# Optimization experiments

Hardware: AMD Instinct MI355X
Metric: run time of the kernel (lower is better)

Reference implementation:

```python
import jax, jax.numpy as jnp
import numpy as np

PATCH_NUMS = (10, 20, 30, 40)   # action_dim=10 * (1,2,3,4)
L = sum(PATCH_NUMS)             # 100
FIRST_L = PATCH_NUMS[0]         # 10
C = 768; NH = 12; HD = C // NH; DEPTH = 8; V = 4096; CVAE = 32; OBS = 23; TO = 1
EPS = 1e-6
STD = 0.02

LVL = np.concatenate([np.full(pn, i, dtype=np.int64) for i, pn in enumerate(PATCH_NUMS)])  # [L]
ATTN_BIAS = np.where(LVL[:, None] >= LVL[None, :], 0.0, -np.inf).astype(np.float32)       # [L, L] block-causal


def _ln(x):
    # LayerNorm without affine (eps=1e-6), as in norm_layer(..., elementwise_affine=False)
    m = x.mean(-1, keepdims=True)
    v = ((x - m) ** 2).mean(-1, keepdims=True)
    return (x - m) / jnp.sqrt(v + EPS)


def setup_inputs() -> dict:
    key = jax.random.key(0)
    ks = iter(jax.random.split(key, 40))
    B = 128
    p = {}
    p["nobs"] = jax.random.normal(next(ks), (B, TO, OBS), jnp.float32)
    p["x_BLCv_wo_first_l"] = jax.random.normal(next(ks), (B, L - FIRST_L, CVAE), jnp.float32)
    p["obs_w"] = jax.random.normal(next(ks), (OBS * TO, C), jnp.float32) * STD
    p["obs_b"] = jnp.zeros((C,), jnp.float32)
    p["word_w"] = jax.random.normal(next(ks), (CVAE, C), jnp.float32) * STD
    p["word_b"] = jnp.zeros((C,), jnp.float32)
    p["pos_start"] = jax.random.normal(next(ks), (1, FIRST_L, C), jnp.float32) * STD
    p["pos_1LC"] = jax.random.normal(next(ks), (1, L, C), jnp.float32) * STD
    p["lvl_emb"] = jax.random.normal(next(ks), (len(PATCH_NUMS), C), jnp.float32) * STD
    p["ada_w"] = jax.random.normal(next(ks), (DEPTH, C, 6 * C), jnp.float32) * STD
    p["ada_b"] = jnp.zeros((DEPTH, 6 * C), jnp.float32)
    p["qkv_w"] = jax.random.normal(next(ks), (DEPTH, C, 3 * C), jnp.float32) * STD
    p["qkv_b"] = jnp.zeros((DEPTH, 3 * C), jnp.float32)
    p["proj_w"] = jax.random.normal(next(ks), (DEPTH, C, C), jnp.float32) * STD
    p["proj_b"] = jnp.zeros((DEPTH, C), jnp.float32)
    p["fc1_w"] = jax.random.normal(next(ks), (DEPTH, C, 4 * C), jnp.float32) * STD
    p["fc1_b"] = jnp.zeros((DEPTH, 4 * C), jnp.float32)
    p["fc2_w"] = jax.random.normal(next(ks), (DEPTH, 4 * C, C), jnp.float32) * STD
    p["fc2_b"] = jnp.zeros((DEPTH, C), jnp.float32)
    p["hnm_w"] = jax.random.normal(next(ks), (C, 2 * C), jnp.float32) * STD
    p["hnm_b"] = jnp.zeros((2 * C,), jnp.float32)
    p["head_w"] = jax.random.normal(next(ks), (C, V), jnp.float32) * STD
    p["head_b"] = jnp.zeros((V,), jnp.float32)
    return p


def reference(nobs, x_BLCv_wo_first_l, obs_w, obs_b, word_w, word_b, pos_start, pos_1LC,
              lvl_emb, ada_w, ada_b, qkv_w, qkv_b, proj_w, proj_b, fc1_w, fc1_b,
              fc2_w, fc2_b, hnm_w, hnm_b, head_w, head_b):
    B = x_BLCv_wo_first_l.shape[0]
    feat = nobs[:, :TO].reshape(B, -1)                     # [B, obs_dim*To]
    cond = feat @ obs_w + obs_b                            # [B, C] (= sos = cond_BD)
    sos = cond[:, None, :] + pos_start                     # [B, first_l, C]
    x = jnp.concatenate([sos, x_BLCv_wo_first_l @ word_w + word_b], axis=1)  # [B, L, C]
    x = x + lvl_emb[jnp.asarray(LVL)][None] + pos_1LC      # lvl + positional embed
    bias = jnp.asarray(ATTN_BIAS)                          # [L, L]
    cond_s = jax.nn.silu(cond)                             # shared SiLU input to each block's ada_lin
    scale = HD ** -0.5
    for i in range(DEPTH):
        ada = (cond_s @ ada_w[i] + ada_b[i]).reshape(B, 1, 6, C)
        g1, g2, s1, s2, sh1, sh2 = (ada[:, :, j] for j in range(6))
        h = _ln(x) * (s1 + 1.0) + sh1
        qkv = (h @ qkv_w[i] + qkv_b[i]).reshape(B, L, 3, NH, HD)
        q, k, v = qkv[:, :, 0], qkv[:, :, 1], qkv[:, :, 2]
        att = jnp.einsum('bqhd,bkhd->bhqk', q, k) * scale
        att = jax.nn.softmax(att + bias, axis=-1)
        o = jnp.einsum('bhqk,bkhd->bqhd', att, v).reshape(B, L, C)
        x = x + (o @ proj_w[i] + proj_b[i]) * g1
        h = _ln(x) * (s2 + 1.0) + sh2
        h = jax.nn.gelu(h @ fc1_w[i] + fc1_b[i]) @ fc2_w[i] + fc2_b[i]
        x = x + h * g2
    # AdaLNBeforeHead + head
    hd = (cond_s @ hnm_w + hnm_b).reshape(B, 1, 2, C)
    x = _ln(x) * (hd[:, :, 0] + 1.0) + hd[:, :, 1]
    return x @ head_w + head_b                             # [B, L, V]
```

## Files before the change

kernel.cpp:

```cpp
#include <hip/hip_runtime.h>
#include <hip/hip_bf16.h>

typedef unsigned short u16;
typedef unsigned int u32;
typedef __attribute__((ext_vector_type(8))) short bf16x8;
typedef __attribute__((ext_vector_type(4))) float f32x4;

#define GLDS(gptr, lptr) __builtin_amdgcn_global_load_lds( \
    (const __attribute__((address_space(1))) u32*)(gptr), \
    (__attribute__((address_space(3))) u32*)(lptr), 16, 0, 0)

__device__ __forceinline__ float bf2f(u16 x) {
  union { float f; u32 u; } c; c.u = ((u32)x) << 16; return c.f;
}
__device__ __forceinline__ u16 f2bf(float f) {
  union { float f; u32 u; } c; c.f = f;
  u32 u = c.u;
  return (u16)((u + 0x7FFFu + ((u >> 16) & 1u)) >> 16);
}

template<int EPI>
__global__ __launch_bounds__(256)
void gemm_kernel(const u16* __restrict__ A, const u16* __restrict__ Bt,
                 const float* __restrict__ bias,
                 u16* __restrict__ outb, float* __restrict__ outf,
                 float* __restrict__ xres, const float* __restrict__ gate, int gstride,
                 int M, int N, int K)
{
  __shared__ u16 ldsA[2][128 * 32];
  __shared__ u16 ldsB[2][128 * 32];
  const int tid = threadIdx.x;
  const int n0 = blockIdx.x * 128;
  const int m0 = blockIdx.y * 128;
  const int wid = tid >> 6, lane = tid & 63;
  const int wm = wid >> 1, wn = wid & 1;
  const int lr = lane & 15, lg = lane >> 4;

  f32x4 acc[4][4];
  #pragma unroll
  for (int i = 0; i < 4; ++i)
    #pragma unroll
    for (int j = 0; j < 4; ++j)
      acc[i][j] = (f32x4){0.f, 0.f, 0.f, 0.f};

  const int KT = K >> 5;
  int cur = 0;

  #define STAGE(buf, kt) do { \
    int k0_ = (kt) << 5; \
    _Pragma("unroll") \
    for (int iss = 0; iss < 2; ++iss) { \
      int f_ = iss * 256 + tid; \
      int row_ = f_ >> 2, gl_ = f_ & 3; \
      int g_ = gl_ ^ (row_ & 3); \
      GLDS(A + (size_t)(m0 + row_) * K + k0_ + g_ * 8, &ldsA[buf][f_ * 8]); \
      GLDS(Bt + (size_t)(n0 + row_) * K + k0_ + g_ * 8, &ldsB[buf][f_ * 8]); \
    } \
  } while (0)

  STAGE(0, 0);
  __syncthreads();
  for (int kt = 0; kt < KT; ++kt) {
    if (kt + 1 < KT) STAGE(cur ^ 1, kt + 1);
    bf16x8 af[4], bfr[4];
    #pragma unroll
    for (int i = 0; i < 4; ++i) {
      int ra = wm * 64 + i * 16 + lr;
      af[i] = *(const bf16x8*)&ldsA[cur][(ra * 4 + (lg ^ (ra & 3))) * 8];
      int rb = wn * 64 + i * 16 + lr;
      bfr[i] = *(const bf16x8*)&ldsB[cur][(rb * 4 + (lg ^ (rb & 3))) * 8];
    }
    #pragma unroll
    for (int mi = 0; mi < 4; ++mi)
      #pragma unroll
      for (int ni = 0; ni < 4; ++ni)
        acc[mi][ni] = __builtin_amdgcn_mfma_f32_16x16x32_bf16(af[mi], bfr[ni], acc[mi][ni], 0, 0, 0);
    __syncthreads();
    cur ^= 1;
  }
  #undef STAGE

  #pragma unroll
  for (int mi = 0; mi < 4; ++mi) {
    #pragma unroll
    for (int ni = 0; ni < 4; ++ni) {
      int col = n0 + wn * 64 + ni * 16 + lr;
      float bcol = bias[col];
      #pragma unroll
      for (int r = 0; r < 4; ++r) {
        int row = m0 + wm * 64 + mi * 16 + lg * 4 + r;
        float v = acc[mi][ni][r] + bcol;
        size_t idx = (size_t)row * N + col;
        if (EPI == 0) {
          outf[idx] = v;
        } else if (EPI == 1) {
          outb[idx] = f2bf(v);
        } else if (EPI == 2) {
          float t = 0.7978845608028654f * (v + 0.044715f * v * v * v);
          t = fminf(fmaxf(t, -15.f), 15.f);
          float e = __expf(2.f * t);
          float g = 0.5f * v * (1.f + (e - 1.f) / (e + 1.f));
          outb[idx] = f2bf(g);
        } else {
          int bb = row / 100;
          float gt = gate[(size_t)bb * gstride + col];
          xres[idx] += v * gt;
        }
      }
    }
  }
}

__global__ __launch_bounds__(256)
void attn_kernel(const u16* __restrict__ qkv, u16* __restrict__ o)
{
  __shared__ u16 Qs[896 * 8];
  __shared__ u16 Ks[896 * 8];
  __shared__ u16 Vt[1024 * 8];
  __shared__ u16 Pl[4][256 * 8];
  const int tid = threadIdx.x;
  const int b = blockIdx.x / 12;
  const int h = blockIdx.x % 12;
  const int wid = tid >> 6, lane = tid & 63;
  const size_t qbase = (size_t)b * 100 * 2304 + h * 64;

  #pragma unroll
  for (int i = 0; i < 16; ++i)
    ((u32*)Pl)[i * 256 + tid] = 0u;

  for (int it = 0; it < 3; ++it) {
    int idx = it * 256 + tid;
    int row = idx >> 3, gl = idx & 7;
    int g = gl ^ (row & 7);
    int sr = row < 100 ? row : 99;
    const u16* gq = qkv + qbase + (size_t)sr * 2304 + g * 8;
    GLDS(gq, &Qs[idx * 8]);
    GLDS(gq + 768, &Ks[idx * 8]);
  }
  if (tid < 128) {
    int idx = 768 + tid;
    int row = idx >> 3, gl = idx & 7;
    int g = gl ^ (row & 7);
    int sr = row < 100 ? row : 99;
    const u16* gq = qkv + qbase + (size_t)sr * 2304 + g * 8;
    GLDS(gq, &Qs[idx * 8]);
    GLDS(gq + 768, &Ks[idx * 8]);
  }

  for (int it = 0; it < 4; ++it) {
    int idx = it * 256 + tid;
    if (idx < 896) {
      int k = idx >> 3, gd = idx & 7;
      int sk = k < 100 ? k : 99;
      const u16* gv = qkv + qbase + (size_t)sk * 2304 + 1536 + gd * 8;
      u16 vv[8];
      *(uint4*)vv = *(const uint4*)gv;
      #pragma unroll
      for (int e = 0; e < 8; ++e) {
        int d = gd * 8 + e;
        Vt[(d * 16 + ((k >> 3) ^ (d & 15))) * 8 + (k & 7)] = vv[e];
      }
    }
  }
  __syncthreads();

  for (int s = wid; s < 7; s += 4) {
    f32x4 sa[7];
    #pragma unroll
    for (int nt = 0; nt < 7; ++nt) sa[nt] = (f32x4){0.f, 0.f, 0.f, 0.f};
    #pragma unroll
    for (int kk = 0; kk < 2; ++kk) {
      int qrow = s * 16 + (lane & 15);
      int qg = kk * 4 + (lane >> 4);
      bf16x8 qa = *(const bf16x8*)&Qs[(qrow * 8 + (qg ^ (qrow & 7))) * 8];
      #pragma unroll
      for (int nt = 0; nt < 7; ++nt) {
        int krow = nt * 16 + (lane & 15);
        bf16x8 kb = *(const bf16x8*)&Ks[(krow * 8 + (qg ^ (krow & 7))) * 8];
        sa[nt] = __builtin_amdgcn_mfma_f32_16x16x32_bf16(qa, kb, sa[nt], 0, 0, 0);
      }
    }
    float pr[7][4];
    #pragma unroll
    for (int r = 0; r < 4; ++r) {
      int q = s * 16 + (lane >> 4) * 4 + r;
      int kmax = q < 10 ? 10 : q < 30 ? 30 : q < 60 ? 60 : 100;
      float m = -1e30f;
      #pragma unroll
      for (int nt = 0; nt < 7; ++nt) {
        int col = nt * 16 + (lane & 15);
        float sv = (col < kmax) ? sa[nt][r] * 0.125f : -1e30f;
        pr[nt][r] = sv;
        m = fmaxf(m, sv);
      }
      m = fmaxf(m, __shfl_xor(m, 1));
      m = fmaxf(m, __shfl_xor(m, 2));
      m = fmaxf(m, __shfl_xor(m, 4));
      m = fmaxf(m, __shfl_xor(m, 8));
      float sum = 0.f;
      #pragma unroll
      for (int nt = 0; nt < 7; ++nt) {
        float e = (pr[nt][r] > -1e29f) ? __expf(pr[nt][r] - m) : 0.f;
        pr[nt][r] = e;
        sum += e;
      }
      sum += __shfl_xor(sum, 1);
      sum += __shfl_xor(sum, 2);
      sum += __shfl_xor(sum, 4);
      sum += __shfl_xor(sum, 8);
      float inv = 1.f / sum;
      #pragma unroll
      for (int nt = 0; nt < 7; ++nt) pr[nt][r] *= inv;
    }
    #pragma unroll
    for (int nt = 0; nt < 7; ++nt) {
      int cg = nt * 2 + ((lane & 15) >> 3);
      int e = lane & 7;
      #pragma unroll
      for (int r = 0; r < 4; ++r) {
        int row = (lane >> 4) * 4 + r;
        Pl[wid][(row * 16 + (cg ^ row)) * 8 + e] = f2bf(pr[nt][r]);
      }
    }
    asm volatile("s_waitcnt lgkmcnt(0)" ::: "memory");
    f32x4 oa[4];
    #pragma unroll
    for (int i = 0; i < 4; ++i) oa[i] = (f32x4){0.f, 0.f, 0.f, 0.f};
    #pragma unroll
    for (int kk = 0; kk < 4; ++kk) {
      int prow = lane & 15;
      int pg = kk * 4 + (lane >> 4);
      bf16x8 pa = *(const bf16x8*)&Pl[wid][(prow * 16 + (pg ^ prow)) * 8];
      #pragma unroll
      for (int nt = 0; nt < 4; ++nt) {
        int vrow = nt * 16 + (lane & 15);
        bf16x8 vb = *(const bf16x8*)&Vt[(vrow * 16 + (pg ^ (vrow & 15))) * 8];
        oa[nt] = __builtin_amdgcn_mfma_f32_16x16x32_bf16(pa, vb, oa[nt], 0, 0, 0);
      }
    }
    #pragma unroll
    for (int nt = 0; nt < 4; ++nt) {
      int d = nt * 16 + (lane & 15);
      #pragma unroll
      for (int r = 0; r < 4; ++r) {
        int q = s * 16 + (lane >> 4) * 4 + r;
        if (q < 100)
          o[(size_t)(b * 100 + q) * 768 + h * 64 + d] = f2bf(oa[nt][r]);
      }
    }
  }
}

__global__ __launch_bounds__(256)
void transpose_cast(const float* __restrict__ in, u16* __restrict__ out, int K, int N)
{
  __shared__ float tile[32][33];
  size_t zo = (size_t)blockIdx.z * K * N;
  const float* ip = in + zo;
  u16* op = out + zo;
  int n0 = blockIdx.x * 32, k0 = blockIdx.y * 32;
  int tx = threadIdx.x & 31, ty = threadIdx.x >> 5;
  #pragma unroll
  for (int i = 0; i < 32; i += 8)
    tile[ty + i][tx] = ip[(size_t)(k0 + ty + i) * N + n0 + tx];
  __syncthreads();
  #pragma unroll
  for (int i = 0; i < 32; i += 8)
    op[(size_t)(n0 + ty + i) * K + k0 + tx] = f2bf(tile[tx][ty + i]);
}

__global__ __launch_bounds__(256)
void cond_kernel(const float* __restrict__ nobs, const float* __restrict__ obs_w,
                 const float* __restrict__ obs_b, float* __restrict__ cond,
                 u16* __restrict__ cond_s)
{
  int idx = blockIdx.x * 256 + threadIdx.x;
  int b = idx / 768, c = idx - b * 768;
  float acc = obs_b[c];
  #pragma unroll
  for (int i = 0; i < 23; ++i)
    acc += nobs[b * 23 + i] * obs_w[i * 768 + c];
  cond[idx] = acc;
  float sg = acc / (1.f + __expf(-acc));
  cond_s[idx] = f2bf(sg);
}

__global__ __launch_bounds__(256)
void cast_bf16_kernel(const float* __restrict__ in, u16* __restrict__ out, int n)
{
  int idx = blockIdx.x * 256 + threadIdx.x;
  if (idx < n) out[idx] = f2bf(in[idx]);
}

__global__ __launch_bounds__(256)
void build_x_kernel(const float* __restrict__ cond, const float* __restrict__ pos_start,
                    const float* __restrict__ xw, const float* __restrict__ lvl_emb,
                    const float* __restrict__ pos_1LC, float* __restrict__ x)
{
  int idx = blockIdx.x * 256 + threadIdx.x;
  int row = idx / 768, c = idx - row * 768;
  int b = row / 100, l = row - b * 100;
  int lvl = l < 10 ? 0 : l < 30 ? 1 : l < 60 ? 2 : 3;
  float v;
  if (l < 10) v = cond[b * 768 + c] + pos_start[l * 768 + c];
  else        v = xw[(size_t)(b * 90 + (l - 10)) * 768 + c];
  x[idx] = v + lvl_emb[lvl * 768 + c] + pos_1LC[l * 768 + c];
}

__global__ __launch_bounds__(256)
void ln_mod_kernel(const float* __restrict__ x, const float* __restrict__ scale_b,
                   const float* __restrict__ shift_b, int stride, u16* __restrict__ h)
{
  int row = blockIdx.x;
  const float* xr = x + (size_t)row * 768;
  int t = threadIdx.x;
  float v0 = xr[t], v1 = xr[t + 256], v2 = xr[t + 512];
  float s = v0 + v1 + v2;
  float q = v0 * v0 + v1 * v1 + v2 * v2;
  #pragma unroll
  for (int o = 32; o > 0; o >>= 1) {
    s += __shfl_down(s, o);
    q += __shfl_down(q, o);
  }
  __shared__ float red[4][2];
  if ((t & 63) == 0) { red[t >> 6][0] = s; red[t >> 6][1] = q; }
  __syncthreads();
  float S = red[0][0] + red[1][0] + red[2][0] + red[3][0];
  float Q = red[0][1] + red[1][1] + red[2][1] + red[3][1];
  float mean = S * (1.f / 768.f);
  float var = Q * (1.f / 768.f) - mean * mean;
  float rstd = rsqrtf(var + 1e-6f);
  int bb = row / 100;
  const float* sc = scale_b + (size_t)bb * stride;
  const float* sh = shift_b + (size_t)bb * stride;
  u16* hr = h + (size_t)row * 768;
  hr[t]       = f2bf((v0 - mean) * rstd * (1.f + sc[t])       + sh[t]);
  hr[t + 256] = f2bf((v1 - mean) * rstd * (1.f + sc[t + 256]) + sh[t + 256]);
  hr[t + 512] = f2bf((v2 - mean) * rstd * (1.f + sc[t + 512]) + sh[t + 512]);
}

extern "C" void kernel_launch(void* const* d_in, const int* in_sizes, int n_in,
                              void* d_out, int out_size, void* d_ws, size_t ws_size,
                              hipStream_t stream)
{
  (void)in_sizes; (void)n_in; (void)out_size; (void)ws_size;
  const float* nobs      = (const float*)d_in[0];
  const float* xv        = (const float*)d_in[1];
  const float* obs_w     = (const float*)d_in[2];
  const float* obs_b     = (const float*)d_in[3];
  const float* word_w    = (const float*)d_in[4];
  const float* word_b    = (const float*)d_in[5];
  const float* pos_start = (const float*)d_in[6];
  const float* pos_1LC   = (const float*)d_in[7];
  const float* lvl_emb   = (const float*)d_in[8];
  const float* ada_w     = (const float*)d_in[9];
  const float* ada_b     = (const float*)d_in[10];
  const float* qkv_w     = (const float*)d_in[11];
  const float* qkv_b     = (const float*)d_in[12];
  const float* proj_w    = (const float*)d_in[13];
  const float* proj_b    = (const float*)d_in[14];
  const float* fc1_w     = (const float*)d_in[15];
  const float* fc1_b     = (const float*)d_in[16];
  const float* fc2_w     = (const float*)d_in[17];
  const float* fc2_b     = (const float*)d_in[18];
  const float* hnm_w     = (const float*)d_in[19];
  const float* hnm_b     = (const float*)d_in[20];
  const float* head_w    = (const float*)d_in[21];
  const float* head_b    = (const float*)d_in[22];
  float* out = (float*)d_out;

  char* p = (char*)d_ws;
  auto take = [&](size_t bytes) { char* r = p; p += (bytes + 255) & ~(size_t)255; return r; };
  u16* Wword   = (u16*)take((size_t)768 * 32 * 2);
  u16* Wada    = (u16*)take((size_t)8 * 4608 * 768 * 2);
  u16* Wqkv    = (u16*)take((size_t)8 * 2304 * 768 * 2);
  u16* Wproj   = (u16*)take((size_t)8 * 768 * 768 * 2);
  u16* Wfc1    = (u16*)take((size_t)8 * 3072 * 768 * 2);
  u16* Wfc2    = (u16*)take((size_t)8 * 768 * 3072 * 2);
  u16* Whnm    = (u16*)take((size_t)1536 * 768 * 2);
  u16* Whead   = (u16*)take((size_t)4096 * 768 * 2);
  float* condf = (float*)take((size_t)128 * 768 * 4);
  u16* conds   = (u16*)take((size_t)128 * 768 * 2);
  u16* xvb     = (u16*)take((size_t)368640 * 2);
  float* xbuf  = (float*)take((size_t)12800 * 768 * 4);
  u16* hbuf    = (u16*)take((size_t)12800 * 768 * 2);
  float* adab  = (float*)take((size_t)128 * 4608 * 4);
  u16* obuf    = (u16*)take((size_t)12800 * 768 * 2);
  float* hdbuf = (float*)take((size_t)128 * 1536 * 4);
  char* big    = take((size_t)12800 * 3072 * 2);
  float* xw  = (float*)big;
  u16* qkvb  = (u16*)big;
  u16* fc1b  = (u16*)big;

  transpose_cast<<<dim3(24, 1, 1),   256, 0, stream>>>(word_w, Wword, 32, 768);
  transpose_cast<<<dim3(144, 24, 8), 256, 0, stream>>>(ada_w,  Wada,  768, 4608);
  transpose_cast<<<dim3(72, 24, 8),  256, 0, stream>>>(qkv_w,  Wqkv,  768, 2304);
  transpose_cast<<<dim3(24, 24, 8),  256, 0, stream>>>(proj_w, Wproj, 768, 768);
  transpose_cast<<<dim3(96, 24, 8),  256, 0, stream>>>(fc1_w,  Wfc1,  768, 3072);
  transpose_cast<<<dim3(24, 96, 8),  256, 0, stream>>>(fc2_w,  Wfc2,  3072, 768);
  transpose_cast<<<dim3(48, 24, 1),  256, 0, stream>>>(hnm_w,  Whnm,  768, 1536);
  transpose_cast<<<dim3(128, 24, 1), 256, 0, stream>>>(head_w, Whead, 768, 4096);

  cond_kernel<<<384, 256, 0, stream>>>(nobs, obs_w, obs_b, condf, conds);
  cast_bf16_kernel<<<1440, 256, 0, stream>>>(xv, xvb, 368640);
  gemm_kernel<0><<<dim3(6, 90), 256, 0, stream>>>(xvb, Wword, word_b,
      nullptr, xw, nullptr, nullptr, 0, 11520, 768, 32);
  build_x_kernel<<<38400, 256, 0, stream>>>(condf, pos_start, xw, lvl_emb, pos_1LC, xbuf);

  for (int i = 0; i < 8; ++i) {
    gemm_kernel<0><<<dim3(36, 1), 256, 0, stream>>>(conds, Wada + (size_t)i * 4608 * 768,
        ada_b + (size_t)i * 4608, nullptr, adab, nullptr, nullptr, 0, 128, 4608, 768);
    ln_mod_kernel<<<12800, 256, 0, stream>>>(xbuf, adab + 2 * 768, adab + 4 * 768, 4608, hbuf);
    gemm_kernel<1><<<dim3(18, 100), 256, 0, stream>>>(hbuf, Wqkv + (size_t)i * 2304 * 768,
        qkv_b + (size_t)i * 2304, qkvb, nullptr, nullptr, nullptr, 0, 12800, 2304, 768);
    attn_kernel<<<1536, 256, 0, stream>>>(qkvb, obuf);
    gemm_kernel<3><<<dim3(6, 100), 256, 0, stream>>>(obuf, Wproj + (size_t)i * 768 * 768,
        proj_b + (size_t)i * 768, nullptr, nullptr, xbuf, adab + 0 * 768, 4608, 12800, 768, 768);
    ln_mod_kernel<<<12800, 256, 0, stream>>>(xbuf, adab + 3 * 768, adab + 5 * 768, 4608, hbuf);
    gemm_kernel<2><<<dim3(24, 100), 256, 0, stream>>>(hbuf, Wfc1 + (size_t)i * 3072 * 768,
        fc1_b + (size_t)i * 3072, fc1b, nullptr, nullptr, nullptr, 0, 12800, 3072, 768);
    gemm_kernel<3><<<dim3(6, 100), 256, 0, stream>>>(fc1b, Wfc2 + (size_t)i * 768 * 3072,
        fc2_b + (size_t)i * 768, nullptr, nullptr, xbuf, adab + 1 * 768, 4608, 12800, 768, 3072);
  }

  gemm_kernel<0><<<dim3(12, 1), 256, 0, stream>>>(conds, Whnm, hnm_b,
      nullptr, hdbuf, nullptr, nullptr, 0, 128, 1536, 768);
  ln_mod_kernel<<<12800, 256, 0, stream>>>(xbuf, hdbuf, hdbuf + 768, 1536, hbuf);
  gemm_kernel<0><<<dim3(32, 100), 256, 0, stream>>>(hbuf, Whead, head_b,
      nullptr, out, nullptr, nullptr, 0, 12800, 4096, 768);
}
```

Baseline: 3.639 ms.

## Add 256x256-tile double-buffered GEMM with XCD remap; batch all adaLN projections

Adds a new GEMM kernel with 256x256 output tiles, 512 threads, 128KB of dynamic LDS double-buffered through global_load_lds, XCD-aware workgroup remapping and setprio around the MFMA bursts. It replaces the previous GEMM for the QKV, proj, fc1, fc2 and head layers. The goal is more data reuse per tile and better overlap of loads with MFMA work. When the workspace is large enough, the eight per-layer adaLN projections are also computed in one launch before the loop, which removes the small GEMM launches inside it. The risks are lower occupancy and the hipFuncSetAttribute call made on every launch.

```diff
diff --git a/kernel.cpp b/kernel.cpp
--- a/kernel.cpp
+++ b/kernel.cpp
@@ -111,6 +111,170 @@
   }
 }
 
+template<int EPI>
+__global__ __launch_bounds__(512, 2)
+void gemm256_kernel(const u16* __restrict__ A, const u16* __restrict__ Bt,
+                    const float* __restrict__ bias,
+                    u16* __restrict__ outb, float* __restrict__ outf,
+                    float* __restrict__ xres, const float* __restrict__ gate, int gstride,
+                    int M, int N, int K)
+{
+  extern __shared__ u16 lds[];
+  u16* ldsA = lds;
+  u16* ldsB = lds + 32768;
+  const int tid = threadIdx.x;
+  const int nX = N >> 8;
+
+  int nwg = gridDim.x;
+  int orig = blockIdx.x;
+  int q = nwg >> 3, r = nwg & 7;
+  int xcd = orig & 7, jj = orig >> 3;
+  int wg = (xcd < r ? xcd * (q + 1) : r * (q + 1) + (xcd - r) * q) + jj;
+  const int m0 = (wg / nX) << 8;
+  const int n0 = (wg % nX) << 8;
+
+  const int wid = tid >> 6, lane = tid & 63;
+  const int wm = wid >> 2, wn = wid & 3;
+  const int lr = lane & 15, lg = lane >> 4;
+
+  const u16* Ag = A + (size_t)m0 * K;
+  const u16* Bg = Bt + (size_t)n0 * K;
+
+  f32x4 acc[8][4];
+  #pragma unroll
+  for (int i = 0; i < 8; ++i)
+    #pragma unroll
+    for (int j = 0; j < 4; ++j)
+      acc[i][j] = (f32x4){0.f, 0.f, 0.f, 0.f};
+
+  const int KT = K >> 6;
+
+  #define ISSUE(ldsbase, G, buf, t1, kk) do { \
+    int k0_ = ((t1) << 6) + ((kk) << 5); \
+    _Pragma("unroll") \
+    for (int is_ = 0; is_ < 2; ++is_) { \
+      int j_ = is_ * 512 + tid; \
+      int row_ = j_ >> 2, gl_ = j_ & 3; \
+      int gs_ = gl_ ^ (row_ & 3); \
+      GLDS((G) + (size_t)row_ * K + k0_ + gs_ * 8, \
+           (ldsbase) + (((((buf) * 2 + (kk)) << 10)) + j_) * 8); \
+    } \
+  } while (0)
+
+  #define RDA(dst, buf, kk, mf) do { \
+    int r_ = wm * 128 + (mf) * 16 + lr; \
+    dst = *(const bf16x8*)&ldsA[(((((buf) * 2 + (kk)) << 10)) + r_ * 4 + (lg ^ (r_ & 3))) * 8]; \
+  } while (0)
+  #define RDB(dst, buf, kk, nf) do { \
+    int r_ = wn * 64 + (nf) * 16 + lr; \
+    dst = *(const bf16x8*)&ldsB[(((((buf) * 2 + (kk)) << 10)) + r_ * 4 + (lg ^ (r_ & 3))) * 8]; \
+  } while (0)
+
+  ISSUE(ldsA, Ag, 0, 0, 0);
+  ISSUE(ldsB, Bg, 0, 0, 0);
+  ISSUE(ldsA, Ag, 0, 0, 1);
+  ISSUE(ldsB, Bg, 0, 0, 1);
+
+  for (int t = 0; t < KT; ++t) {
+    const int c = t & 1;
+    const bool pf = (t + 1) < KT;
+    bf16x8 af[4], bv[4];
+
+    asm volatile("s_waitcnt vmcnt(4)" ::: "memory");
+    __builtin_amdgcn_s_barrier();
+    if (pf) { ISSUE(ldsA, Ag, c ^ 1, t + 1, 0); }
+    RDA(af[0], c, 0, 0); RDA(af[1], c, 0, 1); RDA(af[2], c, 0, 2); RDA(af[3], c, 0, 3);
+    RDB(bv[0], c, 0, 0); RDB(bv[1], c, 0, 1); RDB(bv[2], c, 0, 2); RDB(bv[3], c, 0, 3);
+    __builtin_amdgcn_s_setprio(1);
+    #pragma unroll
+    for (int i = 0; i < 4; ++i)
+      #pragma unroll
+      for (int j = 0; j < 4; ++j)
+        acc[i][j] = __builtin_amdgcn_mfma_f32_16x16x32_bf16(af[i], bv[j], acc[i][j], 0, 0, 0);
+    __builtin_amdgcn_s_setprio(0);
+
+    __builtin_amdgcn_s_barrier();
+    if (pf) { ISSUE(ldsB, Bg, c ^ 1, t + 1, 0); }
+    RDA(af[0], c, 0, 4); RDA(af[1], c, 0, 5); RDA(af[2], c, 0, 6); RDA(af[3], c, 0, 7);
+    __builtin_amdgcn_s_setprio(1);
+    #pragma unroll
+    for (int i = 0; i < 4; ++i)
+      #pragma unroll
+      for (int j = 0; j < 4; ++j)
+        acc[4 + i][j] = __builtin_amdgcn_mfma_f32_16x16x32_bf16(af[i], bv[j], acc[4 + i][j], 0, 0, 0);
+    __builtin_amdgcn_s_setprio(0);
+
+    if (pf) { asm volatile("s_waitcnt vmcnt(4)" ::: "memory"); }
+    else    { asm volatile("s_waitcnt vmcnt(0)" ::: "memory"); }
+    __builtin_amdgcn_s_barrier();
+    if (pf) { ISSUE(ldsA, Ag, c ^ 1, t + 1, 1); }
+    RDA(af[0], c, 1, 0); RDA(af[1], c, 1, 1); RDA(af[2], c, 1, 2); RDA(af[3], c, 1, 3);
+    RDB(bv[0], c, 1, 0); RDB(bv[1], c, 1, 1); RDB(bv[2], c, 1, 2); RDB(bv[3], c, 1, 3);
+    __builtin_amdgcn_s_setprio(1);
+    #pragma unroll
+    for (int i = 0; i < 4; ++i)
+      #pragma unroll
+      for (int j = 0; j < 4; ++j)
+        acc[i][j] = __builtin_amdgcn_mfma_f32_16x16x32_bf16(af[i], bv[j], acc[i][j], 0, 0, 0);
+    __builtin_amdgcn_s_setprio(0);
+
+    __builtin_amdgcn_s_barrier();
+    if (pf) { ISSUE(ldsB, Bg, c ^ 1, t + 1, 1); }
+    RDA(af[0], c, 1, 4); RDA(af[1], c, 1, 5); RDA(af[2], c, 1, 6); RDA(af[3], c, 1, 7);
+    __builtin_amdgcn_s_setprio(1);
+    #pragma unroll
+    for (int i = 0; i < 4; ++i)
+      #pragma unroll
+      for (int j = 0; j < 4; ++j)
+        acc[4 + i][j] = __builtin_amdgcn_mfma_f32_16x16x32_bf16(af[i], bv[j], acc[4 + i][j], 0, 0, 0);
+    __builtin_amdgcn_s_setprio(0);
+  }
+  #undef ISSUE
+  #undef RDA
+  #undef RDB
+
+  #pragma unroll
+  for (int nf = 0; nf < 4; ++nf) {
+    int col = n0 + wn * 64 + nf * 16 + lr;
+    float bcol = bias[col];
+    #pragma unroll
+    for (int mf = 0; mf < 8; ++mf) {
+      #pragma unroll
+      for (int r = 0; r < 4; ++r) {
+        int row = m0 + wm * 128 + mf * 16 + lg * 4 + r;
+        float v = acc[mf][nf][r] + bcol;
+        size_t idx = (size_t)row * N + col;
+        if (EPI == 0) {
+          outf[idx] = v;
+        } else if (EPI == 1) {
+          outb[idx] = f2bf(v);
+        } else if (EPI == 2) {
+          float tg = 0.7978845608028654f * (v + 0.044715f * v * v * v);
+          tg = fminf(fmaxf(tg, -15.f), 15.f);
+          float e = __expf(2.f * tg);
+          float g = 0.5f * v * (1.f + (e - 1.f) / (e + 1.f));
+          outb[idx] = f2bf(g);
+        } else {
+          int bb = row / 100;
+          float gt = gate[(size_t)bb * gstride + col];
+          xres[idx] += v * gt;
+        }
+      }
+    }
+  }
+}
+
+template<int E>
+static inline void launch256(const u16* A, const u16* Bt, const float* bias,
+                             u16* ob, float* of, float* xr, const float* gt, int gs,
+                             int M, int N, int K, hipStream_t s)
+{
+  hipFuncSetAttribute(reinterpret_cast<const void*>(&gemm256_kernel<E>),
+                      hipFuncAttributeMaxDynamicSharedMemorySize, 131072);
+  int nwg = (M >> 8) * (N >> 8);
+  gemm256_kernel<E><<<nwg, 512, 131072, s>>>(A, Bt, bias, ob, of, xr, gt, gs, M, N, K);
+}
+
 __global__ __launch_bounds__(256)
 void attn_kernel(const u16* __restrict__ qkv, u16* __restrict__ o)
 {
@@ -183,8 +347,8 @@
     float pr[7][4];
     #pragma unroll
     for (int r = 0; r < 4; ++r) {
-      int q = s * 16 + (lane >> 4) * 4 + r;
-      int kmax = q < 10 ? 10 : q < 30 ? 30 : q < 60 ? 60 : 100;
+      int qq = s * 16 + (lane >> 4) * 4 + r;
+      int kmax = qq < 10 ? 10 : qq < 30 ? 30 : qq < 60 ? 60 : 100;
       float m = -1e30f;
       #pragma unroll
       for (int nt = 0; nt < 7; ++nt) {
@@ -243,9 +407,9 @@
       int d = nt * 16 + (lane & 15);
       #pragma unroll
       for (int r = 0; r < 4; ++r) {
-        int q = s * 16 + (lane >> 4) * 4 + r;
-        if (q < 100)
-          o[(size_t)(b * 100 + q) * 768 + h * 64 + d] = f2bf(oa[nt][r]);
+        int qq = s * 16 + (lane >> 4) * 4 + r;
+        if (qq < 100)
+          o[(size_t)(b * 100 + qq) * 768 + h * 64 + d] = f2bf(oa[nt][r]);
       }
     }
   }
@@ -316,14 +480,14 @@
   int t = threadIdx.x;
   float v0 = xr[t], v1 = xr[t + 256], v2 = xr[t + 512];
   float s = v0 + v1 + v2;
-  float q = v0 * v0 + v1 * v1 + v2 * v2;
+  float qv = v0 * v0 + v1 * v1 + v2 * v2;
   #pragma unroll
   for (int o = 32; o > 0; o >>= 1) {
     s += __shfl_down(s, o);
-    q += __shfl_down(q, o);
+    qv += __shfl_down(qv, o);
   }
   __shared__ float red[4][2];
-  if ((t & 63) == 0) { red[t >> 6][0] = s; red[t >> 6][1] = q; }
+  if ((t & 63) == 0) { red[t >> 6][0] = s; red[t >> 6][1] = qv; }
   __syncthreads();
   float S = red[0][0] + red[1][0] + red[2][0] + red[3][0];
   float Q = red[0][1] + red[1][1] + red[2][1] + red[3][1];
@@ -343,7 +507,7 @@
                               void* d_out, int out_size, void* d_ws, size_t ws_size,
                               hipStream_t stream)
 {
-  (void)in_sizes; (void)n_in; (void)out_size; (void)ws_size;
+  (void)in_sizes; (void)n_in; (void)out_size;
   const float* nobs      = (const float*)d_in[0];
   const float* xv        = (const float*)d_in[1];
   const float* obs_w     = (const float*)d_in[2];
@@ -369,6 +533,10 @@
   const float* head_b    = (const float*)d_in[22];
   float* out = (float*)d_out;
 
+  const size_t NEED_BIG = 358000000;
+  const bool bigAda = ws_size >= NEED_BIG;
+  const int adaStride = bigAda ? 36864 : 4608;
+
   char* p = (char*)d_ws;
   auto take = [&](size_t bytes) { char* r = p; p += (bytes + 255) & ~(size_t)255; return r; };
   u16* Wword   = (u16*)take((size_t)768 * 32 * 2);
@@ -384,7 +552,7 @@
   u16* xvb     = (u16*)take((size_t)368640 * 2);
   float* xbuf  = (float*)take((size_t)12800 * 768 * 4);
   u16* hbuf    = (u16*)take((size_t)12800 * 768 * 2);
-  float* adab  = (float*)take((size_t)128 * 4608 * 4);
+  float* adab  = (float*)take((size_t)128 * (size_t)adaStride * 4);
   u16* obuf    = (u16*)take((size_t)12800 * 768 * 2);
   float* hdbuf = (float*)take((size_t)128 * 1536 * 4);
   char* big    = take((size_t)12800 * 3072 * 2);
@@ -407,25 +575,31 @@
       nullptr, xw, nullptr, nullptr, 0, 11520, 768, 32);
   build_x_kernel<<<38400, 256, 0, stream>>>(condf, pos_start, xw, lvl_emb, pos_1LC, xbuf);
 
+  if (bigAda)
+    gemm_kernel<0><<<dim3(288, 1), 256, 0, stream>>>(conds, Wada, ada_b,
+        nullptr, adab, nullptr, nullptr, 0, 128, 36864, 768);
+
   for (int i = 0; i < 8; ++i) {
-    gemm_kernel<0><<<dim3(36, 1), 256, 0, stream>>>(conds, Wada + (size_t)i * 4608 * 768,
-        ada_b + (size_t)i * 4608, nullptr, adab, nullptr, nullptr, 0, 128, 4608, 768);
-    ln_mod_kernel<<<12800, 256, 0, stream>>>(xbuf, adab + 2 * 768, adab + 4 * 768, 4608, hbuf);
-    gemm_kernel<1><<<dim3(18, 100), 256, 0, stream>>>(hbuf, Wqkv + (size_t)i * 2304 * 768,
-        qkv_b + (size_t)i * 2304, qkvb, nullptr, nullptr, nullptr, 0, 12800, 2304, 768);
+    if (!bigAda)
+      gemm_kernel<0><<<dim3(36, 1), 256, 0, stream>>>(conds, Wada + (size_t)i * 4608 * 768,
+          ada_b + (size_t)i * 4608, nullptr, adab, nullptr, nullptr, 0, 128, 4608, 768);
+    float* adaL = bigAda ? adab + (size_t)i * 4608 : adab;
+    ln_mod_kernel<<<12800, 256, 0, stream>>>(xbuf, adaL + 2 * 768, adaL + 4 * 768, adaStride, hbuf);
+    launch256<1>(hbuf, Wqkv + (size_t)i * 2304 * 768, qkv_b + (size_t)i * 2304,
+                 qkvb, nullptr, nullptr, nullptr, 0, 12800, 2304, 768, stream);
     attn_kernel<<<1536, 256, 0, stream>>>(qkvb, obuf);
-    gemm_kernel<3><<<dim3(6, 100), 256, 0, stream>>>(obuf, Wproj + (size_t)i * 768 * 768,
-        proj_b + (size_t)i * 768, nullptr, nullptr, xbuf, adab + 0 * 768, 4608, 12800, 768, 768);
-    ln_mod_kernel<<<12800, 256, 0, stream>>>(xbuf, adab + 3 * 768, adab + 5 * 768, 4608, hbuf);
-    gemm_kernel<2><<<dim3(24, 100), 256, 0, stream>>>(hbuf, Wfc1 + (size_t)i * 3072 * 768,
-        fc1_b + (size_t)i * 3072, fc1b, nullptr, nullptr, nullptr, 0, 12800, 3072, 768);
-    gemm_kernel<3><<<dim3(6, 100), 256, 0, stream>>>(fc1b, Wfc2 + (size_t)i * 768 * 3072,
-        fc2_b + (size_t)i * 768, nullptr, nullptr, xbuf, adab + 1 * 768, 4608, 12800, 768, 3072);
+    launch256<3>(obuf, Wproj + (size_t)i * 768 * 768, proj_b + (size_t)i * 768,
+                 nullptr, nullptr, xbuf, adaL + 0 * 768, adaStride, 12800, 768, 768, stream);
+    ln_mod_kernel<<<12800, 256, 0, stream>>>(xbuf, adaL + 3 * 768, adaL + 5 * 768, adaStride, hbuf);
+    launch256<2>(hbuf, Wfc1 + (size_t)i * 3072 * 768, fc1_b + (size_t)i * 3072,
+                 fc1b, nullptr, nullptr, nullptr, 0, 12800, 3072, 768, stream);
+    launch256<3>(fc1b, Wfc2 + (size_t)i * 768 * 3072, fc2_b + (size_t)i * 768,
+                 nullptr, nullptr, xbuf, adaL + 1 * 768, adaStride, 12800, 768, 3072, stream);
   }
 
   gemm_kernel<0><<<dim3(12, 1), 256, 0, stream>>>(conds, Whnm, hnm_b,
       nullptr, hdbuf, nullptr, nullptr, 0, 128, 1536, 768);
   ln_mod_kernel<<<12800, 256, 0, stream>>>(xbuf, hdbuf, hdbuf + 768, 1536, hbuf);
-  gemm_kernel<0><<<dim3(32, 100), 256, 0, stream>>>(hbuf, Whead, head_b,
-      nullptr, out, nullptr, nullptr, 0, 12800, 4096, 768);
-}
+  launch256<0>(hbuf, Whead, head_b, nullptr, out, nullptr, nullptr, 0,
+               12800, 4096, 768, stream);
+}
```

After: 3.719 ms. +2.2%, slower.
